# Optimization experiments

Measured on AMD Instinct MI355X. Metric: run time of the kernel, lower is better.

Reference implementation:

```python
import jax, jax.numpy as jnp
import numpy as np

EMBED = 1024
MLP = 2048
N_EXPERTS = 8
TOP_K = 2


def setup_inputs() -> dict:
    key = jax.random.key(0)
    ks = jax.random.split(key, 5)
    scale_e = 1.0 / np.sqrt(EMBED)
    scale_m = 1.0 / np.sqrt(MLP)
    x = jax.random.normal(ks[0], (4, 2048, EMBED), dtype=jnp.float32)
    gate_w = jax.random.normal(ks[1], (EMBED, N_EXPERTS), dtype=jnp.float32) * scale_e
    w1 = jax.random.normal(ks[2], (N_EXPERTS, EMBED, MLP), dtype=jnp.float32) * scale_e
    w3 = jax.random.normal(ks[3], (N_EXPERTS, EMBED, MLP), dtype=jnp.float32) * scale_e
    w2 = jax.random.normal(ks[4], (N_EXPERTS, MLP, EMBED), dtype=jnp.float32) * scale_m
    return {"x": x, "gate_w": gate_w, "w1": w1, "w2": w2, "w3": w3}


def reference(x, gate_w, w1, w2, w3):
    B, S, D = x.shape
    xf = x.reshape(-1, D)  # [T, D] tokens
    # Router: softmax over experts, top-k select, renormalize selected weights
    router_logits = xf @ gate_w                      # [T, E]
    routing_weights = jax.nn.softmax(router_logits, axis=-1)
    sel_w, sel_e = jax.lax.top_k(routing_weights, TOP_K)  # [T, K]
    sel_w = sel_w / jnp.sum(sel_w, axis=-1, keepdims=True)
    out = jnp.zeros_like(xf)
    # Loop over the small fixed expert set; tokens not routed to expert e get
    # coefficient 0, matching the gather/scatter-add combine of the original.
    for e in range(N_EXPERTS):
        coef = jnp.sum(jnp.where(sel_e == e, sel_w, 0.0), axis=-1)  # [T]
        h = jax.nn.silu(xf @ w1[e]) * (xf @ w3[e])                  # [T, Mlp] SwiGLU
        out = out + coef[:, None] * (h @ w2[e])                     # [T, D]
    return out.reshape(B, S, D)
```

## Files before the change

### kernel.cpp

```cpp
#include <hip/hip_runtime.h>

#define EMBED 1024
#define MLP   2048
#define NE    8
#define NTOK  8192
#define RMAX  (2*NTOK + NE*128)

typedef _Float16 f16x8 __attribute__((ext_vector_type(8)));
typedef _Float16 f16x4 __attribute__((ext_vector_type(4)));
typedef float    f32x4 __attribute__((ext_vector_type(4)));

__global__ __launch_bounds__(256) void router_kernel(
    const float* __restrict__ x, const float* __restrict__ gw,
    int* __restrict__ sel_e, float* __restrict__ sel_w, int* __restrict__ counts)
{
  __shared__ float gwt[NE * EMBED];
  __shared__ int cnt[NE];
  int tid = threadIdx.x;
  for (int idx = tid; idx < NE * EMBED; idx += 256) {
    int i = idx >> 3, e = idx & 7;
    gwt[e * EMBED + i] = gw[idx];
  }
  if (tid < NE) cnt[tid] = 0;
  __syncthreads();

  int lane = tid & 63, wv = tid >> 6;
  int t = blockIdx.x * 4 + wv;
  const float4* xr = (const float4*)(x + (size_t)t * EMBED);
  const float4* gt4 = (const float4*)gwt;
  float acc[NE];
  #pragma unroll
  for (int e = 0; e < NE; ++e) acc[e] = 0.f;
  #pragma unroll
  for (int c = 0; c < 4; ++c) {
    float4 xv = xr[c * 64 + lane];
    #pragma unroll
    for (int e = 0; e < NE; ++e) {
      float4 gv = gt4[e * 256 + c * 64 + lane];
      acc[e] += xv.x * gv.x + xv.y * gv.y + xv.z * gv.z + xv.w * gv.w;
    }
  }
  #pragma unroll
  for (int off = 1; off < 64; off <<= 1) {
    #pragma unroll
    for (int e = 0; e < NE; ++e) acc[e] += __shfl_xor(acc[e], off);
  }
  if (lane == 0) {
    int e0 = 0; float l0 = acc[0];
    #pragma unroll
    for (int e = 1; e < NE; ++e) if (acc[e] > l0) { l0 = acc[e]; e0 = e; }
    int e1 = -1; float l1 = -1e30f;
    #pragma unroll
    for (int e = 0; e < NE; ++e) if (e != e0 && acc[e] > l1) { l1 = acc[e]; e1 = e; }
    float w0 = 1.f / (1.f + expf(l1 - l0));
    sel_e[2 * t] = e0;     sel_w[2 * t] = w0;
    sel_e[2 * t + 1] = e1; sel_w[2 * t + 1] = 1.f - w0;
    atomicAdd(&cnt[e0], 1); atomicAdd(&cnt[e1], 1);
  }
  __syncthreads();
  if (tid < NE && cnt[tid]) atomicAdd(&counts[tid], cnt[tid]);
}

__global__ void offsets_kernel(const int* __restrict__ counts,
                               int* __restrict__ offs, int* __restrict__ cursor)
{
  if (threadIdx.x == 0) {
    int o = 0;
    for (int e = 0; e < NE; ++e) {
      offs[e] = o; cursor[e] = o;
      o += (counts[e] + 127) & ~127;
    }
    offs[NE] = o;
  }
}

__global__ __launch_bounds__(256) void assign_kernel(
    const int* __restrict__ sel_e, const float* __restrict__ sel_w,
    int* __restrict__ cursor, int* __restrict__ rowtok, float* __restrict__ rowcoef)
{
  int t = blockIdx.x * 256 + threadIdx.x;
  int lane = threadIdx.x & 63;
  #pragma unroll
  for (int k = 0; k < 2; ++k) {
    int e = sel_e[2 * t + k];
    float w = sel_w[2 * t + k];
    for (int xch = 0; xch < NE; ++xch) {
      unsigned long long m = __ballot(e == xch);
      if (e == xch) {
        int leader = __ffsll((unsigned long long)m) - 1;
        int base = 0;
        if (lane == leader) base = atomicAdd(&cursor[xch], (int)__popcll(m));
        base = __shfl(base, leader);
        int pos = base + (int)__popcll(m & ((1ull << lane) - 1));
        rowtok[pos] = t;
        rowcoef[pos] = w;
      }
    }
  }
}

__global__ __launch_bounds__(256) void gather_kernel(
    const float* __restrict__ x, const int* __restrict__ rowtok,
    _Float16* __restrict__ xg)
{
  int r = blockIdx.x;
  int tok = rowtok[r];
  int t4 = threadIdx.x * 4;
  _Float16* dst = xg + (size_t)r * EMBED + t4;
  if (tok >= 0) {
    float4 v = *(const float4*)(x + (size_t)tok * EMBED + t4);
    f16x4 h; h.x = (_Float16)v.x; h.y = (_Float16)v.y; h.z = (_Float16)v.z; h.w = (_Float16)v.w;
    *(f16x4*)dst = h;
  } else {
    f16x4 z = {(_Float16)0.f, (_Float16)0.f, (_Float16)0.f, (_Float16)0.f};
    *(f16x4*)dst = z;
  }
}

__global__ __launch_bounds__(256) void transpose_cast_kernel(
    const float* __restrict__ in, _Float16* __restrict__ out, int K, int N)
{
  const float* src = in + (size_t)blockIdx.z * K * N;
  _Float16* dst = out + (size_t)blockIdx.z * K * N;
  int k0 = blockIdx.x * 64, n0 = blockIdx.y * 64;
  __shared__ float tile[64][65];
  int t = threadIdx.x;
  int r = t >> 4, c4 = (t & 15) * 4;
  #pragma unroll
  for (int i = 0; i < 4; ++i) {
    float4 v = *(const float4*)(src + (size_t)(k0 + r + 16 * i) * N + n0 + c4);
    tile[r + 16 * i][c4 + 0] = v.x;
    tile[r + 16 * i][c4 + 1] = v.y;
    tile[r + 16 * i][c4 + 2] = v.z;
    tile[r + 16 * i][c4 + 3] = v.w;
  }
  __syncthreads();
  int kk8 = (t & 7) * 8, nIdx = t >> 3;
  #pragma unroll
  for (int i = 0; i < 2; ++i) {
    int n = nIdx + 32 * i;
    f16x8 h;
    #pragma unroll
    for (int j = 0; j < 8; ++j) h[j] = (_Float16)tile[kk8 + j][n];
    *(f16x8*)(dst + (size_t)(n0 + n) * K + k0 + kk8) = h;
  }
}

__device__ __forceinline__ int resolve_expert(const int* __restrict__ offs, int r0)
{
  int e = 0;
  #pragma unroll
  for (int q = 0; q < NE - 1; ++q) if (r0 >= offs[q + 1]) e = q + 1;
  return e;
}

__global__ __launch_bounds__(256, 2) void gemm1_kernel(
    const _Float16* __restrict__ xg, const _Float16* __restrict__ w1t,
    const _Float16* __restrict__ w3t, const float* __restrict__ rowcoef,
    const int* __restrict__ offs, _Float16* __restrict__ hb)
{
  int r0 = blockIdx.x * 128;
  if (r0 >= offs[NE]) return;
  int e = resolve_expert(offs, r0);
  int n0 = blockIdx.y * 128;
  const _Float16* B1 = w1t + (size_t)e * MLP * EMBED;
  const _Float16* B3 = w3t + (size_t)e * MLP * EMBED;

  __shared__ __align__(16) _Float16 As[128 * 32];
  __shared__ __align__(16) _Float16 Bs1[128 * 32];
  __shared__ __align__(16) _Float16 Bs3[128 * 32];

  int tid = threadIdx.x, lane = tid & 63, wv = tid >> 6;
  int wm = (wv & 1) << 6, wn = (wv >> 1) << 6;
  int l16 = lane & 15, quad = lane >> 4;

  f32x4 acc1[4][4], acc3[4][4];
  f32x4 z4 = {0.f, 0.f, 0.f, 0.f};
  #pragma unroll
  for (int i = 0; i < 4; ++i)
    #pragma unroll
    for (int j = 0; j < 4; ++j) { acc1[i][j] = z4; acc3[i][j] = z4; }

  for (int kk = 0; kk < EMBED; kk += 32) {
    __syncthreads();
    #pragma unroll
    for (int p = 0; p < 2; ++p) {
      int c = p * 256 + tid;
      int row = c >> 2, kp = (c & 3) << 3;
      *(f16x8*)(As  + c * 8) = *(const f16x8*)(xg + (size_t)(r0 + row) * EMBED + kk + kp);
      *(f16x8*)(Bs1 + c * 8) = *(const f16x8*)(B1 + (size_t)(n0 + row) * EMBED + kk + kp);
      *(f16x8*)(Bs3 + c * 8) = *(const f16x8*)(B3 + (size_t)(n0 + row) * EMBED + kk + kp);
    }
    __syncthreads();
    f16x8 af[4], b1f[4], b3f[4];
    #pragma unroll
    for (int i = 0; i < 4; ++i)
      af[i] = *(const f16x8*)(As + (wm + 16 * i + l16) * 32 + quad * 8);
    #pragma unroll
    for (int j = 0; j < 4; ++j) {
      b1f[j] = *(const f16x8*)(Bs1 + (wn + 16 * j + l16) * 32 + quad * 8);
      b3f[j] = *(const f16x8*)(Bs3 + (wn + 16 * j + l16) * 32 + quad * 8);
    }
    #pragma unroll
    for (int i = 0; i < 4; ++i)
      #pragma unroll
      for (int j = 0; j < 4; ++j) {
        acc1[i][j] = __builtin_amdgcn_mfma_f32_16x16x32_f16(af[i], b1f[j], acc1[i][j], 0, 0, 0);
        acc3[i][j] = __builtin_amdgcn_mfma_f32_16x16x32_f16(af[i], b3f[j], acc3[i][j], 0, 0, 0);
      }
  }

  #pragma unroll
  for (int i = 0; i < 4; ++i) {
    int mb = r0 + wm + 16 * i + quad * 4;
    float cf[4];
    #pragma unroll
    for (int rg = 0; rg < 4; ++rg) cf[rg] = rowcoef[mb + rg];
    #pragma unroll
    for (int j = 0; j < 4; ++j) {
      int col = n0 + wn + 16 * j + l16;
      #pragma unroll
      for (int rg = 0; rg < 4; ++rg) {
        float g = acc1[i][j][rg], u = acc3[i][j][rg];
        float h = g * u * cf[rg] / (1.f + __expf(-g));
        hb[(size_t)(mb + rg) * MLP + col] = (_Float16)h;
      }
    }
  }
}

__global__ __launch_bounds__(256, 2) void gemm2_kernel(
    const _Float16* __restrict__ hb, const _Float16* __restrict__ w2t,
    const int* __restrict__ rowtok, const int* __restrict__ offs,
    float* __restrict__ out)
{
  int r0 = blockIdx.x * 128;
  if (r0 >= offs[NE]) return;
  int e = resolve_expert(offs, r0);
  int n0 = blockIdx.y * 128;
  const _Float16* B = w2t + (size_t)e * EMBED * MLP;

  __shared__ __align__(16) _Float16 As[128 * 32];
  __shared__ __align__(16) _Float16 Bs[128 * 32];

  int tid = threadIdx.x, lane = tid & 63, wv = tid >> 6;
  int wm = (wv & 1) << 6, wn = (wv >> 1) << 6;
  int l16 = lane & 15, quad = lane >> 4;

  f32x4 acc[4][4];
  f32x4 z4 = {0.f, 0.f, 0.f, 0.f};
  #pragma unroll
  for (int i = 0; i < 4; ++i)
    #pragma unroll
    for (int j = 0; j < 4; ++j) acc[i][j] = z4;

  for (int kk = 0; kk < MLP; kk += 32) {
    __syncthreads();
    #pragma unroll
    for (int p = 0; p < 2; ++p) {
      int c = p * 256 + tid;
      int row = c >> 2, kp = (c & 3) << 3;
      *(f16x8*)(As + c * 8) = *(const f16x8*)(hb + (size_t)(r0 + row) * MLP + kk + kp);
      *(f16x8*)(Bs + c * 8) = *(const f16x8*)(B  + (size_t)(n0 + row) * MLP + kk + kp);
    }
    __syncthreads();
    f16x8 af[4], bf[4];
    #pragma unroll
    for (int i = 0; i < 4; ++i)
      af[i] = *(const f16x8*)(As + (wm + 16 * i + l16) * 32 + quad * 8);
    #pragma unroll
    for (int j = 0; j < 4; ++j)
      bf[j] = *(const f16x8*)(Bs + (wn + 16 * j + l16) * 32 + quad * 8);
    #pragma unroll
    for (int i = 0; i < 4; ++i)
      #pragma unroll
      for (int j = 0; j < 4; ++j)
        acc[i][j] = __builtin_amdgcn_mfma_f32_16x16x32_f16(af[i], bf[j], acc[i][j], 0, 0, 0);
  }

  #pragma unroll
  for (int i = 0; i < 4; ++i) {
    int mb = r0 + wm + 16 * i + quad * 4;
    int tk[4];
    #pragma unroll
    for (int rg = 0; rg < 4; ++rg) tk[rg] = rowtok[mb + rg];
    #pragma unroll
    for (int j = 0; j < 4; ++j) {
      int col = n0 + wn + 16 * j + l16;
      #pragma unroll
      for (int rg = 0; rg < 4; ++rg)
        if (tk[rg] >= 0)
          atomicAdd(out + (size_t)tk[rg] * EMBED + col, acc[i][j][rg]);
    }
  }
}

extern "C" void kernel_launch(void* const* d_in, const int* in_sizes, int n_in,
                              void* d_out, int out_size, void* d_ws, size_t ws_size,
                              hipStream_t stream)
{
  (void)in_sizes; (void)n_in; (void)ws_size;
  const float* x  = (const float*)d_in[0];
  const float* gw = (const float*)d_in[1];
  const float* w1 = (const float*)d_in[2];
  const float* w2 = (const float*)d_in[3];
  const float* w3 = (const float*)d_in[4];
  float* out = (float*)d_out;
  char* ws = (char*)d_ws;

  size_t o = 0;
  auto alloc = [&](size_t bytes) { size_t r = o; o = (o + bytes + 255) & ~255ULL; return r; };
  const size_t wbytes = (size_t)NE * MLP * EMBED * 2;
  _Float16* w1t = (_Float16*)(ws + alloc(wbytes));
  _Float16* w3t = (_Float16*)(ws + alloc(wbytes));
  _Float16* w2t = (_Float16*)(ws + alloc(wbytes));
  _Float16* xg  = (_Float16*)(ws + alloc((size_t)RMAX * EMBED * 2));
  _Float16* hb  = (_Float16*)(ws + alloc((size_t)RMAX * MLP * 2));
  int*   rowtok  = (int*)(ws + alloc((size_t)RMAX * 4));
  float* rowcoef = (float*)(ws + alloc((size_t)RMAX * 4));
  int*   sel_e   = (int*)(ws + alloc((size_t)2 * NTOK * 4));
  float* sel_w   = (float*)(ws + alloc((size_t)2 * NTOK * 4));
  int*   meta    = (int*)(ws + alloc(256));
  int* counts = meta;
  int* offs   = meta + 8;
  int* cursor = meta + 17;

  hipMemsetAsync(out, 0, (size_t)out_size * 4, stream);
  hipMemsetAsync(meta, 0, 256, stream);
  hipMemsetAsync(rowtok, 0xFF, (size_t)RMAX * 4, stream);
  hipMemsetAsync(rowcoef, 0, (size_t)RMAX * 4, stream);

  transpose_cast_kernel<<<dim3(EMBED / 64, MLP / 64, NE), 256, 0, stream>>>(w1, w1t, EMBED, MLP);
  transpose_cast_kernel<<<dim3(EMBED / 64, MLP / 64, NE), 256, 0, stream>>>(w3, w3t, EMBED, MLP);
  transpose_cast_kernel<<<dim3(MLP / 64, EMBED / 64, NE), 256, 0, stream>>>(w2, w2t, MLP, EMBED);

  router_kernel<<<NTOK / 4, 256, 0, stream>>>(x, gw, sel_e, sel_w, counts);
  offsets_kernel<<<1, 64, 0, stream>>>(counts, offs, cursor);
  assign_kernel<<<NTOK / 256, 256, 0, stream>>>(sel_e, sel_w, cursor, rowtok, rowcoef);
  gather_kernel<<<RMAX, 256, 0, stream>>>(x, rowtok, xg);

  gemm1_kernel<<<dim3(RMAX / 128, MLP / 128), 256, 0, stream>>>(xg, w1t, w3t, rowcoef, offs, hb);
  gemm2_kernel<<<dim3(RMAX / 128, EMBED / 128), 256, 0, stream>>>(hb, w2t, rowtok, offs, out);
}
```

Before: 698.5 us.

## Use direct global-to-LDS loads with XOR-swizzled tiles in both expert GEMMs

Replaces the register-staged global-to-shared tile copies in both grouped GEMM kernels with global_load_lds 16-byte direct copies, which skip the VGPR round trip. The shared tile layout gets an XOR swizzle on the k-quad index, and the fragment reads use the matching address function to cut LDS bank conflicts. Relies on global_load_lds 16-byte support on this architecture and on the wave-contiguous LDS destination layout matching the swizzle. There is still no double buffering, so load latency is only partly hidden.

```diff
diff --git a/kernel.cpp b/kernel.cpp
--- a/kernel.cpp
+++ b/kernel.cpp
@@ -9,6 +9,12 @@
 typedef _Float16 f16x8 __attribute__((ext_vector_type(8)));
 typedef _Float16 f16x4 __attribute__((ext_vector_type(4)));
 typedef float    f32x4 __attribute__((ext_vector_type(4)));
+
+__device__ __forceinline__ void async_copy16(const void* g, void* l) {
+  __builtin_amdgcn_global_load_lds(
+      (const __attribute__((address_space(1))) unsigned int*)g,
+      (__attribute__((address_space(3))) unsigned int*)l, 16, 0, 0);
+}
 
 __global__ __launch_bounds__(256) void router_kernel(
     const float* __restrict__ x, const float* __restrict__ gw,
@@ -154,6 +160,11 @@
   return e;
 }
 
+__device__ __forceinline__ const _Float16* frag_addr(const _Float16* buf, int row, int quad)
+{
+  return buf + row * 32 + ((quad ^ ((row >> 1) & 3)) << 3);
+}
+
 __global__ __launch_bounds__(256, 2) void gemm1_kernel(
     const _Float16* __restrict__ xg, const _Float16* __restrict__ w1t,
     const _Float16* __restrict__ w3t, const float* __restrict__ rowcoef,
@@ -186,20 +197,24 @@
     #pragma unroll
     for (int p = 0; p < 2; ++p) {
       int c = p * 256 + tid;
-      int row = c >> 2, kp = (c & 3) << 3;
-      *(f16x8*)(As  + c * 8) = *(const f16x8*)(xg + (size_t)(r0 + row) * EMBED + kk + kp);
-      *(f16x8*)(Bs1 + c * 8) = *(const f16x8*)(B1 + (size_t)(n0 + row) * EMBED + kk + kp);
-      *(f16x8*)(Bs3 + c * 8) = *(const f16x8*)(B3 + (size_t)(n0 + row) * EMBED + kk + kp);
+      int row = c >> 2, kqp = c & 3;
+      int kql = kqp ^ ((row >> 1) & 3);
+      size_t gof = (size_t)(r0 + row) * EMBED + kk + kql * 8;
+      size_t gofB = (size_t)(n0 + row) * EMBED + kk + kql * 8;
+      int lof = (p * 256 + wv * 64) * 8;
+      async_copy16(xg + gof,  As  + lof);
+      async_copy16(B1 + gofB, Bs1 + lof);
+      async_copy16(B3 + gofB, Bs3 + lof);
     }
     __syncthreads();
     f16x8 af[4], b1f[4], b3f[4];
     #pragma unroll
     for (int i = 0; i < 4; ++i)
-      af[i] = *(const f16x8*)(As + (wm + 16 * i + l16) * 32 + quad * 8);
+      af[i] = *(const f16x8*)frag_addr(As, wm + 16 * i + l16, quad);
     #pragma unroll
     for (int j = 0; j < 4; ++j) {
-      b1f[j] = *(const f16x8*)(Bs1 + (wn + 16 * j + l16) * 32 + quad * 8);
-      b3f[j] = *(const f16x8*)(Bs3 + (wn + 16 * j + l16) * 32 + quad * 8);
+      b1f[j] = *(const f16x8*)frag_addr(Bs1, wn + 16 * j + l16, quad);
+      b3f[j] = *(const f16x8*)frag_addr(Bs3, wn + 16 * j + l16, quad);
     }
     #pragma unroll
     for (int i = 0; i < 4; ++i)
@@ -259,18 +274,22 @@
     #pragma unroll
     for (int p = 0; p < 2; ++p) {
       int c = p * 256 + tid;
-      int row = c >> 2, kp = (c & 3) << 3;
-      *(f16x8*)(As + c * 8) = *(const f16x8*)(hb + (size_t)(r0 + row) * MLP + kk + kp);
-      *(f16x8*)(Bs + c * 8) = *(const f16x8*)(B  + (size_t)(n0 + row) * MLP + kk + kp);
+      int row = c >> 2, kqp = c & 3;
+      int kql = kqp ^ ((row >> 1) & 3);
+      size_t gofA = (size_t)(r0 + row) * MLP + kk + kql * 8;
+      size_t gofB = (size_t)(n0 + row) * MLP + kk + kql * 8;
+      int lof = (p * 256 + wv * 64) * 8;
+      async_copy16(hb + gofA, As + lof);
+      async_copy16(B  + gofB, Bs + lof);
     }
     __syncthreads();
     f16x8 af[4], bf[4];
     #pragma unroll
     for (int i = 0; i < 4; ++i)
-      af[i] = *(const f16x8*)(As + (wm + 16 * i + l16) * 32 + quad * 8);
+      af[i] = *(const f16x8*)frag_addr(As, wm + 16 * i + l16, quad);
     #pragma unroll
     for (int j = 0; j < 4; ++j)
-      bf[j] = *(const f16x8*)(Bs + (wn + 16 * j + l16) * 32 + quad * 8);
+      bf[j] = *(const f16x8*)frag_addr(Bs, wn + 16 * j + l16, quad);
     #pragma unroll
     for (int i = 0; i < 4; ++i)
       #pragma unroll
```

After: 678.4 us. -2.9%, faster.
